# Optimization experiments

Hardware: AMD Instinct MI355X
Metric: run time of the kernel (lower is better)

Reference implementation:

```python
import jax, jax.numpy as jnp
import numpy as np

RADIUS = [1.0, 1.5, 2.0, 100.0]  # bucket boundaries; last is catch-all
NFILT = len(RADIUS)
C_IN, C_OUT = 256, 512


def setup_inputs() -> dict:
    key = jax.random.key(0)
    k1, k2, k3, k4 = jax.random.split(key, 4)
    b, n = 16, 4096
    feat = jax.random.normal(k1, (b, n, C_IN), dtype=jnp.float32)
    xyz = jax.random.normal(k2, (b, n, 3), dtype=jnp.float32)
    # init per original reset_parameters
    std = 2.0 * np.sqrt(2.0 / (C_IN + C_OUT))
    a = np.sqrt(3.0) * std
    weight = jax.random.uniform(k3, (NFILT, C_OUT, C_IN), dtype=jnp.float32, minval=-a, maxval=a)
    bound = 1.0 / np.sqrt(C_IN)
    bias = jax.random.uniform(k4, (NFILT, C_OUT), dtype=jnp.float32, minval=-bound, maxval=bound)
    return {"feat": feat, "xyz": xyz, "weight": weight, "bias": bias}


def reference(feat, xyz, weight, bias):
    b, n, c = feat.shape
    p = feat.reshape(b * n, c)                      # (P, C)
    radii = jnp.asarray(RADIUS, dtype=feat.dtype)
    r_norm = jnp.linalg.norm(xyz.reshape(b * n, 3), axis=1)
    # first radius with r_norm < r (same as the sequential break in map2filtId)
    filt_id = jnp.argmax(r_norm[:, None] < radii[None, :], axis=1)  # (P,)
    # grouped linear expressed densely: all Nfilt GEMMs, then per-point select
    all_out = jnp.einsum('pc,foc->fpo', p, weight) + bias[:, None, :]  # (F, P, O)
    out = jnp.take_along_axis(all_out, filt_id[None, :, None], axis=0)[0]  # (P, O)
    return out.reshape(b, n, -1)
```

## Files before the change

### kernel.cpp

```cpp
#include <hip/hip_runtime.h>
#include <hip/hip_bf16.h>

#define C_IN   256
#define C_OUT  512
#define NFILT  4

#define BM 128
#define BN 128
#define BK 32
#define SAS 40

#define FBK 64

typedef __attribute__((ext_vector_type(8))) short bf16x8;
typedef __attribute__((ext_vector_type(4))) float floatx4;

union Pack8 { uint4 u; __hip_bfloat16 h[8]; };

__global__ __launch_bounds__(1024) void bucketize_kernel(
    const float* __restrict__ xyz, int* __restrict__ idxbuf,
    int* __restrict__ cnt, int P)
{
    __shared__ int hist[NFILT];
    __shared__ int wbase[16][NFILT];
    __shared__ int gbase[NFILT];

    int tid = threadIdx.x;
    int wid = tid >> 6;
    int lane = tid & 63;
    if (tid < NFILT) hist[tid] = 0;
    __syncthreads();

    int pid = blockIdx.x * 1024 + tid;
    int filt = -1;
    if (pid < P) {
        float x = xyz[pid * 3 + 0];
        float y = xyz[pid * 3 + 1];
        float z = xyz[pid * 3 + 2];
        float r2 = __fadd_rn(__fadd_rn(__fmul_rn(x, x), __fmul_rn(y, y)), __fmul_rn(z, z));
        float r = sqrtf(r2);
        if (r < 1.0f)        filt = 0;
        else if (r < 1.5f)   filt = 1;
        else if (r < 2.0f)   filt = 2;
        else if (r < 100.0f) filt = 3;
        else                 filt = 0;
    }

    int myoff = 0;
#pragma unroll
    for (int f = 0; f < NFILT; ++f) {
        unsigned long long m = __ballot(filt == f);
        if (lane == 0) wbase[wid][f] = atomicAdd(&hist[f], (int)__popcll(m));
        if (filt == f) myoff = __popcll(m & ((1ull << lane) - 1ull));
    }
    __syncthreads();
    if (tid < NFILT) gbase[tid] = atomicAdd(&cnt[tid], hist[tid]);
    __syncthreads();

    if (filt >= 0)
        idxbuf[filt * P + gbase[filt] + wbase[wid][filt] + myoff] = pid;
}

__global__ void convert_w_kernel(const float* __restrict__ w,
                                 ushort* __restrict__ wb,
                                 int* __restrict__ cnt) {
    if (blockIdx.x == 0 && threadIdx.x < NFILT) cnt[threadIdx.x] = 0;
    int i = (blockIdx.x * blockDim.x + threadIdx.x) * 4;
    float4 v = *(const float4*)(w + i);
    union { ushort4 u; __hip_bfloat16 h[4]; } cv;
    cv.h[0] = __float2bfloat16(v.x);
    cv.h[1] = __float2bfloat16(v.y);
    cv.h[2] = __float2bfloat16(v.z);
    cv.h[3] = __float2bfloat16(v.w);
    *(ushort4*)(wb + i) = cv.u;
}

__global__ __launch_bounds__(256) void gather_kernel(
    const float* __restrict__ feat, const int* __restrict__ idxbuf,
    const int* __restrict__ cnt, ushort* __restrict__ gA, int P)
{
    int wid = threadIdx.x >> 6;
    int lane = threadIdx.x & 63;
    int slot = blockIdx.x * 4 + wid;
    if (slot >= P) return;
    int c0 = cnt[0], c1 = cnt[1], c2 = cnt[2];
    int b1 = c0, b2 = c0 + c1, b3 = c0 + c1 + c2;
    int f, i;
    if (slot < b1)      { f = 0; i = slot; }
    else if (slot < b2) { f = 1; i = slot - b1; }
    else if (slot < b3) { f = 2; i = slot - b2; }
    else                { f = 3; i = slot - b3; }
    int pid = idxbuf[f * P + i];
    float4 v = *(const float4*)(feat + (size_t)pid * C_IN + lane * 4);
    union { ushort4 u; __hip_bfloat16 h[4]; } cv;
    cv.h[0] = __float2bfloat16(v.x);
    cv.h[1] = __float2bfloat16(v.y);
    cv.h[2] = __float2bfloat16(v.z);
    cv.h[3] = __float2bfloat16(v.w);
    *(ushort4*)(gA + (size_t)slot * C_IN + lane * 4) = cv.u;
}

#define STAGE(s, b) do {                                                        \
    int kByte = (s) * (FBK * 2);                                                \
    _Pragma("unroll")                                                           \
    for (int n = 0; n < 4; ++n) {                                               \
        int seg = wid * 4 + n;                                                  \
        int row = seg * 8 + lrow;                                               \
        const char* srcA = aBase + ((size_t)(gBase + row) * (C_IN * 2))         \
                                 + kByte + schunk * 16;                         \
        __builtin_amdgcn_global_load_lds(                                       \
            (const __attribute__((address_space(1))) void*)srcA,                \
            (__attribute__((address_space(3))) void*)&sA[b][seg * 512], 16, 0, 0); \
        const char* srcB = bBase + ((size_t)(wRow0 + row) * (C_IN * 2))         \
                                 + kByte + schunk * 16;                         \
        __builtin_amdgcn_global_load_lds(                                       \
            (const __attribute__((address_space(1))) void*)srcB,                \
            (__attribute__((address_space(3))) void*)&sB[b][seg * 512], 16, 0, 0); \
    }                                                                           \
} while (0)

__global__ __launch_bounds__(256) void gemm_fast_kernel(
    const ushort* __restrict__ gA, const ushort* __restrict__ wb,
    const float* __restrict__ bias, const int* __restrict__ idxbuf,
    const int* __restrict__ cnt, float* __restrict__ out, int P)
{
    __shared__ ushort sA[2][BM * FBK];
    __shared__ ushort sB[2][BN * FBK];
    __shared__ int    sIdx[BM];
    __shared__ float  sBias[BN];

    int lid = blockIdx.x + (blockIdx.y << 2);
    int g = lid & 7;
    int q = lid >> 3;
    int cTile = q & 3;
    int t = ((q >> 2) << 3) + g;

    int c0 = cnt[0], c1 = cnt[1], c2 = cnt[2], c3 = cnt[3];
    int counts[4] = {c0, c1, c2, c3};
    int bases[4]  = {0, c0, c0 + c1, c0 + c1 + c2};
    int f = -1, lt = 0;
    for (int ff = 0; ff < 4; ++ff) {
        int nt = (counts[ff] + BM - 1) / BM;
        if (t < nt) { f = ff; lt = t; break; }
        t -= nt;
    }
    if (f < 0) return;

    int tid = threadIdx.x;
    int oBase = cTile * BN;
    int cn = counts[f];
    int gBase = bases[f] + lt * BM;
    int wRow0 = f * C_OUT + oBase;

    int wid = tid >> 6;
    int lane = tid & 63;
    int wm = (wid >> 1) * 64;
    int wn = (wid & 1) * 64;
    int lcol = lane & 15;
    int quad = lane >> 4;
    int rp = lcol & 7;

    int lrow = lane >> 3;
    int lchunk = lane & 7;
    int schunk = lchunk ^ lrow;

    const char* aBase = (const char*)gA;
    const char* bBase = (const char*)wb;

    STAGE(0, 0);
    if (tid < BM) {
        int r = lt * BM + tid;
        sIdx[tid] = (r < cn) ? idxbuf[f * P + r] : -1;
    }
    if (tid < BN) sBias[tid] = bias[f * C_OUT + oBase + tid];
    __syncthreads();

    floatx4 acc[4][4];
#pragma unroll
    for (int i = 0; i < 4; ++i)
#pragma unroll
        for (int j = 0; j < 4; ++j)
            acc[i][j] = (floatx4){0.f, 0.f, 0.f, 0.f};

#pragma unroll
    for (int s = 0; s < C_IN / FBK; ++s) {
        if (s < C_IN / FBK - 1) STAGE(s + 1, (s + 1) & 1);

        const ushort* cA = sA[s & 1];
        const ushort* cB = sB[s & 1];
#pragma unroll
        for (int kk2 = 0; kk2 < 2; ++kk2) {
            int ck = ((kk2 * 4 + quad) ^ rp) * 8;
            bf16x8 af[4], bfr[4];
#pragma unroll
            for (int i = 0; i < 4; ++i)
                af[i] = *(const bf16x8*)&cA[(wm + i * 16 + lcol) * FBK + ck];
#pragma unroll
            for (int j = 0; j < 4; ++j)
                bfr[j] = *(const bf16x8*)&cB[(wn + j * 16 + lcol) * FBK + ck];
#pragma unroll
            for (int i = 0; i < 4; ++i)
#pragma unroll
                for (int j = 0; j < 4; ++j)
                    acc[i][j] = __builtin_amdgcn_mfma_f32_16x16x32_bf16(af[i], bfr[j], acc[i][j], 0, 0, 0);
        }

        asm volatile("s_waitcnt vmcnt(0)" ::: "memory");
        __builtin_amdgcn_s_barrier();
        __builtin_amdgcn_sched_barrier(0);
    }

#pragma unroll
    for (int i = 0; i < 4; ++i) {
        int r0 = wm + i * 16 + quad * 4;
        int pid0 = sIdx[r0 + 0];
        int pid1 = sIdx[r0 + 1];
        int pid2 = sIdx[r0 + 2];
        int pid3 = sIdx[r0 + 3];
#pragma unroll
        for (int j = 0; j < 4; ++j) {
            int o = oBase + wn + j * 16 + lcol;
            float bv = sBias[wn + j * 16 + lcol];
            if (pid0 >= 0) out[pid0 * C_OUT + o] = acc[i][j][0] + bv;
            if (pid1 >= 0) out[pid1 * C_OUT + o] = acc[i][j][1] + bv;
            if (pid2 >= 0) out[pid2 * C_OUT + o] = acc[i][j][2] + bv;
            if (pid3 >= 0) out[pid3 * C_OUT + o] = acc[i][j][3] + bv;
        }
    }
}

__global__ __launch_bounds__(256) void gemm_kernel(
    const float* __restrict__ feat, const ushort* __restrict__ wb,
    const float* __restrict__ bias, const int* __restrict__ idxbuf,
    const int* __restrict__ cnt, float* __restrict__ out, int P)
{
    __shared__ ushort sA[BM * SAS];
    __shared__ ushort sB[BN * SAS];
    __shared__ int    sIdx[BM];
    __shared__ float  sBias[BN];

    int lid = blockIdx.x + (blockIdx.y << 2);
    int g = lid & 7;
    int q = lid >> 3;
    int cTile = q & 3;
    int t = ((q >> 2) << 3) + g;

    int counts[4];
    counts[0] = cnt[0]; counts[1] = cnt[1]; counts[2] = cnt[2]; counts[3] = cnt[3];
    int f = -1, lt = 0;
    for (int ff = 0; ff < 4; ++ff) {
        int nt = (counts[ff] + BM - 1) / BM;
        if (t < nt) { f = ff; lt = t; break; }
        t -= nt;
    }
    if (f < 0) return;

    int tid = threadIdx.x;
    int oBase = cTile * BN;
    int rowBase = lt * BM;
    int cn = counts[f];

    if (tid < BM) {
        int r = rowBase + tid;
        sIdx[tid] = (r < cn) ? idxbuf[f * P + r] : -1;
    }
    if (tid < BN) sBias[tid] = bias[f * C_OUT + oBase + tid];
    __syncthreads();

    int sRow = tid >> 1;
    int sHalf = tid & 1;
    int myIdx = sIdx[sRow];
    const float* aRow = feat + (size_t)(myIdx < 0 ? 0 : myIdx) * C_IN + sHalf * 16;
    const ushort* bRow = wb + (size_t)(f * C_OUT + oBase + sRow) * C_IN + sHalf * 16;

    int wid = tid >> 6;
    int lane = tid & 63;
    int wm = (wid >> 1) * 64;
    int wn = (wid & 1) * 64;
    int lcol = lane & 15;
    int quad = lane >> 4;

    floatx4 acc[4][4];
#pragma unroll
    for (int i = 0; i < 4; ++i)
#pragma unroll
        for (int j = 0; j < 4; ++j)
            acc[i][j] = (floatx4){0.f, 0.f, 0.f, 0.f};

    for (int kk = 0; kk < C_IN; kk += BK) {
        const float* ap = aRow + kk;
        float4 a0 = *(const float4*)(ap + 0);
        float4 a1 = *(const float4*)(ap + 4);
        float4 a2 = *(const float4*)(ap + 8);
        float4 a3 = *(const float4*)(ap + 12);
        const ushort* bp = bRow + kk;
        uint4 b01 = *(const uint4*)(bp + 0);
        uint4 b23 = *(const uint4*)(bp + 8);

        Pack8 p0, p1;
        p0.h[0] = __float2bfloat16(a0.x); p0.h[1] = __float2bfloat16(a0.y);
        p0.h[2] = __float2bfloat16(a0.z); p0.h[3] = __float2bfloat16(a0.w);
        p0.h[4] = __float2bfloat16(a1.x); p0.h[5] = __float2bfloat16(a1.y);
        p0.h[6] = __float2bfloat16(a1.z); p0.h[7] = __float2bfloat16(a1.w);
        p1.h[0] = __float2bfloat16(a2.x); p1.h[1] = __float2bfloat16(a2.y);
        p1.h[2] = __float2bfloat16(a2.z); p1.h[3] = __float2bfloat16(a2.w);
        p1.h[4] = __float2bfloat16(a3.x); p1.h[5] = __float2bfloat16(a3.y);
        p1.h[6] = __float2bfloat16(a3.z); p1.h[7] = __float2bfloat16(a3.w);

        ushort* dA = &sA[sRow * SAS + sHalf * 16];
        *(uint4*)(dA + 0) = p0.u;
        *(uint4*)(dA + 8) = p1.u;
        ushort* dB = &sB[sRow * SAS + sHalf * 16];
        *(uint4*)(dB + 0) = b01;
        *(uint4*)(dB + 8) = b23;

        __syncthreads();

        bf16x8 af[4], bfr[4];
#pragma unroll
        for (int i = 0; i < 4; ++i)
            af[i] = *(const bf16x8*)&sA[(wm + i * 16 + lcol) * SAS + quad * 8];
#pragma unroll
        for (int j = 0; j < 4; ++j)
            bfr[j] = *(const bf16x8*)&sB[(wn + j * 16 + lcol) * SAS + quad * 8];
#pragma unroll
        for (int i = 0; i < 4; ++i)
#pragma unroll
            for (int j = 0; j < 4; ++j)
                acc[i][j] = __builtin_amdgcn_mfma_f32_16x16x32_bf16(af[i], bfr[j], acc[i][j], 0, 0, 0);

        __syncthreads();
    }

#pragma unroll
    for (int i = 0; i < 4; ++i) {
        int r0 = wm + i * 16 + quad * 4;
        int pid0 = sIdx[r0 + 0];
        int pid1 = sIdx[r0 + 1];
        int pid2 = sIdx[r0 + 2];
        int pid3 = sIdx[r0 + 3];
#pragma unroll
        for (int j = 0; j < 4; ++j) {
            int o = oBase + wn + j * 16 + lcol;
            float bv = sBias[wn + j * 16 + lcol];
            if (pid0 >= 0) out[pid0 * C_OUT + o] = acc[i][j][0] + bv;
            if (pid1 >= 0) out[pid1 * C_OUT + o] = acc[i][j][1] + bv;
            if (pid2 >= 0) out[pid2 * C_OUT + o] = acc[i][j][2] + bv;
            if (pid3 >= 0) out[pid3 * C_OUT + o] = acc[i][j][3] + bv;
        }
    }
}

extern "C" void kernel_launch(void* const* d_in, const int* in_sizes, int n_in,
                              void* d_out, int out_size, void* d_ws, size_t ws_size,
                              hipStream_t stream) {
    const float* feat = (const float*)d_in[0];
    const float* xyz  = (const float*)d_in[1];
    const float* w    = (const float*)d_in[2];
    const float* bias = (const float*)d_in[3];
    float* out = (float*)d_out;
    int P = in_sizes[0] / C_IN;

    char* ws = (char*)d_ws;
    size_t offIdx = 0;
    size_t offCnt = (size_t)4 * P * 4;
    size_t offWb  = offCnt + 16;
    size_t offGA  = (offWb + (size_t)NFILT * C_OUT * C_IN * 2 + 255) & ~(size_t)255;
    size_t needed = offGA + (size_t)(P + BM) * C_IN * 2;

    int* idxbuf = (int*)(ws + offIdx);
    int* cntp   = (int*)(ws + offCnt);
    ushort* wb  = (ushort*)(ws + offWb);

    convert_w_kernel<<<(NFILT * C_OUT * C_IN) / 1024, 256, 0, stream>>>(w, wb, cntp);
    bucketize_kernel<<<(P + 1023) / 1024, 1024, 0, stream>>>(xyz, idxbuf, cntp, P);

    int tilesY = ((P / BM + NFILT + 7) / 8) * 8;
    dim3 grid(C_OUT / BN, tilesY);

    if (ws_size >= needed) {
        ushort* gA = (ushort*)(ws + offGA);
        gather_kernel<<<(P + 3) / 4, 256, 0, stream>>>(feat, idxbuf, cntp, gA, P);
        gemm_fast_kernel<<<grid, 256, 0, stream>>>(gA, wb, bias, idxbuf, cntp, out, P);
    } else {
        gemm_kernel<<<grid, 256, 0, stream>>>(feat, wb, bias, idxbuf, cntp, out, P);
    }
}
```

Before: 233.8 us.

## Halve GEMM K-stage to 32 and raise occupancy with smaller LDS tiles

Cuts the per-stage K depth of the grouped bf16 GEMM from 64 to 32, halving LDS buffers, and reworks the swizzle for the new row width. It adds launch_bounds min-blocks 4 and a sched_barrier after issuing loads, so more workgroups can be resident per CU to hide global-load latency. In exchange there are twice as many pipeline steps and barriers, and less MFMA work per synchronisation.

```diff
diff --git a/kernel.cpp b/kernel.cpp
--- a/kernel.cpp
+++ b/kernel.cpp
@@ -10,7 +10,7 @@
 #define BK 32
 #define SAS 40
 
-#define FBK 64
+#define NSTEP 8
 
 typedef __attribute__((ext_vector_type(8))) short bf16x8;
 typedef __attribute__((ext_vector_type(4))) float floatx4;
@@ -100,12 +100,12 @@
     *(ushort4*)(gA + (size_t)slot * C_IN + lane * 4) = cv.u;
 }
 
-#define STAGE(s, b) do {                                                        \
-    int kByte = (s) * (FBK * 2);                                                \
+#define STAGE32(s, b) do {                                                      \
+    int kByte = (s) * 64;                                                       \
     _Pragma("unroll")                                                           \
-    for (int n = 0; n < 4; ++n) {                                               \
-        int seg = wid * 4 + n;                                                  \
-        int row = seg * 8 + lrow;                                               \
+    for (int n = 0; n < 2; ++n) {                                               \
+        int seg = wid * 2 + n;                             \
+        int row = seg * 16 + (lane >> 2);                                       \
         const char* srcA = aBase + ((size_t)(gBase + row) * (C_IN * 2))         \
                                  + kByte + schunk * 16;                         \
         __builtin_amdgcn_global_load_lds(                                       \
@@ -119,13 +119,13 @@
     }                                                                           \
 } while (0)
 
-__global__ __launch_bounds__(256) void gemm_fast_kernel(
+__global__ __launch_bounds__(256, 4) void gemm_fast_kernel(
     const ushort* __restrict__ gA, const ushort* __restrict__ wb,
     const float* __restrict__ bias, const int* __restrict__ idxbuf,
     const int* __restrict__ cnt, float* __restrict__ out, int P)
 {
-    __shared__ ushort sA[2][BM * FBK];
-    __shared__ ushort sB[2][BN * FBK];
+    __shared__ ushort sA[2][BM * 32];
+    __shared__ ushort sB[2][BN * 32];
     __shared__ int    sIdx[BM];
     __shared__ float  sBias[BN];
 
@@ -158,16 +158,15 @@
     int wn = (wid & 1) * 64;
     int lcol = lane & 15;
     int quad = lane >> 4;
-    int rp = lcol & 7;
-
-    int lrow = lane >> 3;
-    int lchunk = lane & 7;
-    int schunk = lchunk ^ lrow;
+
+    int rchunk = (quad ^ ((lcol >> 1) & 3)) * 8;
+
+    int schunk = (lane & 3) ^ ((lane >> 3) & 3);
 
     const char* aBase = (const char*)gA;
     const char* bBase = (const char*)wb;
 
-    STAGE(0, 0);
+    STAGE32(0, 0);
     if (tid < BM) {
         int r = lt * BM + tid;
         sIdx[tid] = (r < cn) ? idxbuf[f * P + r] : -1;
@@ -183,27 +182,24 @@
             acc[i][j] = (floatx4){0.f, 0.f, 0.f, 0.f};
 
 #pragma unroll
-    for (int s = 0; s < C_IN / FBK; ++s) {
-        if (s < C_IN / FBK - 1) STAGE(s + 1, (s + 1) & 1);
+    for (int s = 0; s < NSTEP; ++s) {
+        if (s < NSTEP - 1) STAGE32(s + 1, (s + 1) & 1);
+        __builtin_amdgcn_sched_barrier(0);
 
         const ushort* cA = sA[s & 1];
         const ushort* cB = sB[s & 1];
-#pragma unroll
-        for (int kk2 = 0; kk2 < 2; ++kk2) {
-            int ck = ((kk2 * 4 + quad) ^ rp) * 8;
-            bf16x8 af[4], bfr[4];
-#pragma unroll
-            for (int i = 0; i < 4; ++i)
-                af[i] = *(const bf16x8*)&cA[(wm + i * 16 + lcol) * FBK + ck];
+        bf16x8 af[4], bfr[4];
+#pragma unroll
+        for (int i = 0; i < 4; ++i)
+            af[i] = *(const bf16x8*)&cA[(wm + i * 16 + lcol) * 32 + rchunk];
+#pragma unroll
+        for (int j = 0; j < 4; ++j)
+            bfr[j] = *(const bf16x8*)&cB[(wn + j * 16 + lcol) * 32 + rchunk];
+#pragma unroll
+        for (int i = 0; i < 4; ++i)
 #pragma unroll
             for (int j = 0; j < 4; ++j)
-                bfr[j] = *(const bf16x8*)&cB[(wn + j * 16 + lcol) * FBK + ck];
-#pragma unroll
-            for (int i = 0; i < 4; ++i)
-#pragma unroll
-                for (int j = 0; j < 4; ++j)
-                    acc[i][j] = __builtin_amdgcn_mfma_f32_16x16x32_bf16(af[i], bfr[j], acc[i][j], 0, 0, 0);
-        }
+                acc[i][j] = __builtin_amdgcn_mfma_f32_16x16x32_bf16(af[i], bfr[j], acc[i][j], 0, 0, 0);
 
         asm volatile("s_waitcnt vmcnt(0)" ::: "memory");
         __builtin_amdgcn_s_barrier();
```

After: 239.3 us. +2.3%, slower.
